# Performance work log

Hardware: AMD Instinct MI355X
Metric: run time of the kernel (lower is better)

Reference implementation:

```python
import jax, jax.numpy as jnp
import numpy as np

# Config matching init_kwargs: input_shape=(C,T,H,W)=(512,32,14,14), window_size=9, n_heads=8
B, C, T, H, W = 2, 512, 32, 14, 14
N, K = 8, 9
CI = C // N              # per-head inter channels (64)
P = (K - 1) // 2         # symmetric temporal zero-pad so S == T


def setup_inputs() -> dict:
    key = jax.random.key(0)
    ks = jax.random.split(key, 7)
    s = 0.02
    return {
        "x":  jax.random.normal(ks[0], (B, C, T, H, W), jnp.float32),
        # per-head 1x1x1 conv (Linear3d) weights/biases, stacked over heads
        "Wq": jax.random.normal(ks[1], (N, CI, C), jnp.float32) * s,
        "bq": jax.random.normal(ks[2], (N, CI), jnp.float32) * s,
        "Wk": jax.random.normal(ks[3], (N, CI, C), jnp.float32) * s,
        "bk": jax.random.normal(ks[4], (N, CI), jnp.float32) * s,
        "Wv": jax.random.normal(ks[5], (N, CI, C), jnp.float32) * s,
        "bv": jax.random.normal(ks[6], (N, CI), jnp.float32) * s,
    }


def reference(x, Wq, bq, Wk, bk, Wv, bv):
    # x: (B, C, T, H, W). Dropout (p=0.25) is inference-mode identity.
    Bx, Cx, Tx, Hx, Wd = x.shape
    HW = Hx * Wd
    xf = x.reshape(Bx, Cx, Tx, HW)

    # Queries: every original frame is the center of its own window -> project x directly.
    q = jnp.einsum('bctp,nic->bnitp', xf, Wq) + bq[None, :, :, None, None]  # (B,N,ci,T,HW)

    # Keys/values on temporally zero-padded input (Pad3d gives S == T windows).
    xp = jnp.pad(xf, ((0, 0), (0, 0), (P, P), (0, 0)))  # (B,C,T+K-1,HW)
    k = jnp.einsum('bctp,nic->bnitp', xp, Wk) + bk[None, :, :, None, None]
    v = jnp.einsum('bctp,nic->bnitp', xp, Wv) + bv[None, :, :, None, None]

    # Sliding windows over padded time: window s covers padded frames s..s+K-1
    win = jnp.arange(Tx)[:, None] + jnp.arange(K)[None, :]  # (T,K)
    kw = k[:, :, :, win]  # (B,N,ci,T,K,HW)
    vw = v[:, :, :, win].reshape(Bx, N, CI, Tx, K * HW)

    # alpha[b,n,t,p,m] = sum_i q[b,n,i,t,p] * k_win[b,n,i,t,m]; softmax over keys m
    alpha = jnp.einsum('bnitp,bnitkm->bntpkm', q, kw).reshape(Bx, N, Tx, HW, K * HW)
    alpha = jax.nn.softmax(alpha, axis=-1)

    # y = alpha @ value -> (B,N,ci,T,HW); head concat is channel-major reshape
    y = jnp.einsum('bntpm,bnitm->bnitp', alpha, vw)
    z = y.reshape(Bx, Cx, Tx, Hx, Wd) + x  # residual
    return z
```

## Files before the change

kernel.cpp:

```cpp
#include <hip/hip_runtime.h>
#include <hip/hip_bf16.h>
#include <stdint.h>
#include <cstddef>

#define BB  2
#define CC  512
#define TT  32
#define HWP 196
#define NH  8
#define KWIN 9
#define CID 64
#define PPAD 4
#define TP  40
#define MTOT 12544
#define NTOT 1536
#define VSLOT 224
#define LOG2E 1.44269504f

typedef unsigned short u16;
typedef unsigned int   u32;
typedef __attribute__((ext_vector_type(8))) short short8;
typedef __attribute__((ext_vector_type(4))) float floatx4;

__device__ __forceinline__ u16 f2bf(float f) {
    u32 u = __float_as_uint(f);
    u32 r = (u + 0x7fffu + ((u >> 16) & 1u)) >> 16;
    return (u16)r;
}
__device__ __forceinline__ u32 pack2bf(float a, float b) {
    return (u32)f2bf(a) | ((u32)f2bf(b) << 16);
}
__device__ __forceinline__ u32 packtrunc(float a, float b) {
    return __builtin_amdgcn_perm(__float_as_uint(b), __float_as_uint(a), 0x07060302u);
}
__device__ __forceinline__ float fexp2(float x) {
    return __builtin_amdgcn_exp2f(x);
}
__device__ __forceinline__ void gload16(const u16* g, u16* l) {
    __builtin_amdgcn_global_load_lds(
        (const __attribute__((address_space(1))) u32*)g,
        (__attribute__((address_space(3))) u32*)l, 16, 0, 0);
}

__global__ __launch_bounds__(256) void prep_transpose(
    const float* __restrict__ x, u16* __restrict__ xt,
    const float* __restrict__ Wq, const float* __restrict__ Wk,
    const float* __restrict__ Wv, u16* __restrict__ Wbf,
    const float* __restrict__ bk, const float* __restrict__ bv,
    u16* __restrict__ Kout, u16* __restrict__ Vtp)
{
    __shared__ float T[64 * 197];
    int bxg = blockIdx.x;
    int tid = threadIdx.x;

    if (bxg < BB * TT * 8) {
        int bx = bxg;
        int ct = bx & 7; bx >>= 3;
        int t = bx & 31;
        int b = bx >> 5;
        const float* src = x + ((size_t)(b * CC + ct * 64) * TT + t) * HWP;
        for (int i = tid; i < 64 * 49; i += 256) {
            int c = i / 49;
            int p4 = i - c * 49;
            float4 v = *(const float4*)(src + (size_t)c * (TT * HWP) + p4 * 4);
            float* Tp = &T[c * 197 + p4 * 4];
            Tp[0] = v.x; Tp[1] = v.y; Tp[2] = v.z; Tp[3] = v.w;
        }
        __syncthreads();
        u16* dst = xt + (size_t)((b * TT + t) * HWP) * CC + ct * 64;
        for (int i = tid; i < HWP * 8; i += 256) {
            int p = i >> 3;
            int c0 = (i & 7) * 8;
            u32 w[4];
            #pragma unroll
            for (int k = 0; k < 4; k++)
                w[k] = pack2bf(T[(c0 + 2 * k) * 197 + p],
                               T[(c0 + 2 * k + 1) * 197 + p]);
            *(uint4*)(dst + (size_t)p * CC + c0) = *(uint4*)w;
        }
        return;
    }

    int id = (bxg - BB * TT * 8) * 256 + tid;
    const int wtot = NTOT * CC / 2;
    const int kper = 2 * NH * 8 * HWP * 32;
    const int vper = 2 * NH * 8 * 64 * (VSLOT/2);
    if (id < wtot) {
        int c2 = id & 255;
        int oc = id >> 8;
        int kind = oc >> 9;
        int idx = oc & 511;
        const float* src = (kind == 0 ? Wq : (kind == 1 ? Wk : Wv)) + (size_t)idx * CC + c2 * 2;
        ((u32*)Wbf)[id] = pack2bf(src[0], src[1]);
    } else if (id < wtot + kper) {
        int i = id - wtot;
        int ci2 = i & 31; i >>= 5;
        int p = i % HWP;  i /= HWP;
        int fr = i & 7;   i >>= 3;
        int head = i & 7;
        int b = i >> 3;
        int tp = fr < 4 ? fr : fr + 32;
        const float* bias = bk + head * CID + ci2 * 2;
        size_t addr = (((size_t)(b * NH + head) * TP + tp) * HWP + p) * 32 + ci2;
        ((u32*)Kout)[addr] = pack2bf(bias[0], bias[1]);
    } else if (id < wtot + kper + vper) {
        int i = id - wtot - kper;
        int s2 = i % (VSLOT/2); i /= (VSLOT/2);
        int ci = i & 63; i >>= 6;
        int fr = i & 7;  i >>= 3;
        int head = i & 7;
        int b = i >> 3;
        int tp = fr < 4 ? fr : fr + 32;
        float bias = bv[head * CID + ci];
        size_t addr = (((size_t)(b * NH + head) * TP + tp) * 64 + ci) * (VSLOT/2) + s2;
        ((u32*)Vtp)[addr] = pack2bf(bias, bias);
    }
}

__global__ __launch_bounds__(512) void proj_gemm2(
    const u16* __restrict__ xt, const u16* __restrict__ Wbf,
    const float* __restrict__ bq, const float* __restrict__ bk,
    const float* __restrict__ bv,
    u16* __restrict__ Qout, u16* __restrict__ Kout, u16* __restrict__ Vtp)
{
    __shared__ u16 sA[128 * 64];
    __shared__ u16 sB[256 * 64];

    int bx = blockIdx.x;
    int nb = bx % 6;
    int mt = bx / 6;
    int tid = threadIdx.x;
    int wave = tid >> 6, lane = tid & 63, quad = lane >> 4, l15 = lane & 15;
    int wm = wave >> 2, wn = wave & 3;
    int mbase = mt * 128 + wm * 64;
    int nbase = nb * 256 + wn * 64;

    int lr = lane >> 3;
    int sw = ((lane & 7) * 8) ^ (lr << 3);

    floatx4 acc[4][4];
    #pragma unroll
    for (int ms = 0; ms < 4; ms++)
        #pragma unroll
        for (int ns = 0; ns < 4; ns++)
            acc[ms][ns] = (floatx4){0.f, 0.f, 0.f, 0.f};

    const u16* abase = xt + (size_t)(mt * 128) * CC;
    const u16* bbase = Wbf + (size_t)(nb * 256) * CC;

    for (int kc = 0; kc < 8; kc++) {
        __syncthreads();
        #pragma unroll
        for (int i = 0; i < 2; i++) {
            int rbase = wave * 16 + i * 8;
            gload16(abase + (size_t)(rbase + lr) * CC + kc * 64 + sw,
                    &sA[rbase * 64]);
        }
        #pragma unroll
        for (int i = 0; i < 4; i++) {
            int rbase = wave * 32 + i * 8;
            gload16(bbase + (size_t)(rbase + lr) * CC + kc * 64 + sw,
                    &sB[rbase * 64]);
        }
        __syncthreads();

        #pragma unroll
        for (int kk = 0; kk < 2; kk++) {
            int swr = (kk * 32 + quad * 8) ^ ((l15 & 7) << 3);
            short8 af[4], bf[4];
            #pragma unroll
            for (int ms = 0; ms < 4; ms++)
                af[ms] = *(const short8*)&sA[(wm * 64 + ms * 16 + l15) * 64 + swr];
            #pragma unroll
            for (int ns = 0; ns < 4; ns++)
                bf[ns] = *(const short8*)&sB[(wn * 64 + ns * 16 + l15) * 64 + swr];
            #pragma unroll
            for (int ms = 0; ms < 4; ms++)
                #pragma unroll
                for (int ns = 0; ns < 4; ns++)
                    acc[ms][ns] = __builtin_amdgcn_mfma_f32_16x16x32_bf16(
                        af[ms], bf[ns], acc[ms][ns], 0, 0, 0);
        }
    }

    float biasv[4];
    #pragma unroll
    for (int ns = 0; ns < 4; ns++) {
        int n = nbase + ns * 16 + l15;
        int kind = n >> 9;
        int idx = n & 511;
        const float* bpb = kind == 0 ? bq : (kind == 1 ? bk : bv);
        biasv[ns] = bpb[idx];
    }

    #pragma unroll
    for (int ms = 0; ms < 4; ms++) {
        #pragma unroll
        for (int r = 0; r < 4; r++) {
            int m = mbase + ms * 16 + quad * 4 + r;
            int b = m / (TT * HWP);
            int rem = m - b * (TT * HWP);
            int t = rem / HWP;
            int p = rem - t * HWP;
            int slot_p = (p & ~31) | (p & 3) | (((p >> 4) & 1) << 2)
                       | (((p >> 2) & 1) << 3) | (((p >> 3) & 1) << 4);
            #pragma unroll
            for (int ns = 0; ns < 4; ns++) {
                int n = nbase + ns * 16 + l15;
                int kind = n >> 9;
                int idx = n & 511;
                int head = idx >> 6;
                int ci = idx & 63;
                float val = acc[ms][ns][r] + biasv[ns];
                if (kind == 0) {
                    Qout[(((size_t)(b * NH + head) * TT + t) * HWP + p) * CID + ci]
                        = f2bf(val * LOG2E);
                } else if (kind == 1) {
                    Kout[(((size_t)(b * NH + head) * TP + (t + PPAD)) * HWP + p) * CID + ci]
                        = f2bf(val);
                } else {
                    Vtp[(((size_t)(b * NH + head) * TP + (t + PPAD)) * 64 + ci) * VSLOT + slot_p]
                        = f2bf(val);
                }
            }
        }
    }
}

__global__ __launch_bounds__(512, 1) void attn_mfma4(
    const float* __restrict__ x,
    const u16* __restrict__ Qb, const u16* __restrict__ Kb,
    const u16* __restrict__ Vtp, float* __restrict__ zout)
{
    __shared__ union {
        struct { u16 K[26 * 512]; u16 V[28 * 512]; } s;
        struct { float eT[192 * 66]; float eT12[4][4][66]; float ls12[4][4]; } e;
    } u;

    int i = blockIdx.x;
    int xcd = i & 7;
    int r = i >> 3;
    int slab = ((r >= 16) ? 8 : 0) | xcd;
    int tpair = r & 15;
    int t0 = tpair * 2;
    int b = slab >> 3, n = slab & 7;

    int tid = threadIdx.x;
    int wave = tid >> 6;
    int grp = wave >> 2;
    int wq = wave & 3;
    int t = t0 + grp;
    int lane = tid & 63;
    int quad = lane >> 4, l15 = lane & 15;
    int lr = lane >> 3;
    int ksw = ((lane & 7) * 8) ^ (lr << 3);

    const u16* kfr0 = Kb + (size_t)slab * (TP * HWP) * CID;
    const u16* vslab = Vtp + (size_t)slab * (TP * 64 * VSLOT);
    const float tmask = (quad == 0) ? 1.0f : 0.0f;

    short8 qf[3][2];
    #pragma unroll
    for (int j = 0; j < 3; j++) {
        int qrow = (wq + 4 * j) * 16 + l15;
        const u16* qp = Qb + ((size_t)(slab * TT + t) * HWP + qrow) * CID;
        qf[j][0] = *(const short8*)(qp + quad * 8);
        qf[j][1] = *(const short8*)(qp + 32 + quad * 8);
    }
    short8 qf12[2];
    {
        int qrow = 192 + l15;
        qrow = qrow < HWP ? qrow : (HWP - 1);
        const u16* qp = Qb + ((size_t)(slab * TT + t) * HWP + qrow) * CID;
        qf12[0] = *(const short8*)(qp + quad * 8);
        qf12[1] = *(const short8*)(qp + 32 + quad * 8);
    }

    floatx4 acc[3][4];
    floatx4 accl[3];
    floatx4 acc12[4];
    floatx4 accl12;
    #pragma unroll
    for (int j = 0; j < 3; j++) {
        #pragma unroll
        for (int cg = 0; cg < 4; cg++) acc[j][cg] = (floatx4){0.f, 0.f, 0.f, 0.f};
        accl[j] = (floatx4){0.f, 0.f, 0.f, 0.f};
    }
    #pragma unroll
    for (int cg = 0; cg < 4; cg++) acc12[cg] = (floatx4){0.f, 0.f, 0.f, 0.f};
    accl12 = (floatx4){0.f, 0.f, 0.f, 0.f};

    union { u32 w[4]; short8 s; } ones;
    ones.w[0] = 0x3F803F80u; ones.w[1] = 0x3F803F80u;
    ones.w[2] = 0x3F803F80u; ones.w[3] = 0x3F803F80u;

    #define KLOAD_L(c, D00, D01, D10, D11) do {                                  \
        int r0_ = (c) * 32 + l15;                                                \
        int sx_ = (l15 & 7) << 3;                                                \
        const u16* a0_ = &u.s.K[r0_ * 64];                                       \
        const u16* a1_ = &u.s.K[(r0_ + 16) * 64];                                \
        D00 = *(const short8*)(a0_ + ((quad * 8) ^ sx_));                        \
        D01 = *(const short8*)(a0_ + ((32 + quad * 8) ^ sx_));                   \
        D10 = *(const short8*)(a1_ + ((quad * 8) ^ sx_));                        \
        D11 = *(const short8*)(a1_ + ((32 + quad * 8) ^ sx_));                   \
    } while (0)

    #define KLOADTAIL_L(D00, D01) do {                                           \
        int r0_ = 192 + l15;                                                     \
        int sx_ = (l15 & 7) << 3;                                                \
        const u16* a0_ = &u.s.K[r0_ * 64];                                       \
        D00 = *(const short8*)(a0_ + ((quad * 8) ^ sx_));                        \
        D01 = *(const short8*)(a0_ + ((32 + quad * 8) ^ sx_));                   \
    } while (0)

    #define VLOAD_L(c, D0, D1, D2, D3) do {                                      \
        const u16* v_ = &u.s.V[l15 * VSLOT + (c) * 32 + quad * 8];               \
        D0 = *(const short8*)(v_);                                               \
        D1 = *(const short8*)(v_ + 16 * VSLOT);                                  \
        D2 = *(const short8*)(v_ + 32 * VSLOT);                                  \
        D3 = *(const short8*)(v_ + 48 * VSLOT);                                  \
    } while (0)

    #define CHUNK_ONE(Q0, Q1, ACC, ACCL, K00, K01, K10, K11, V0, V1, V2, V3) do {\
        floatx4 sc0 = (floatx4){0.f, 0.f, 0.f, 0.f};                             \
        sc0 = __builtin_amdgcn_mfma_f32_16x16x32_bf16(K00, Q0, sc0, 0, 0, 0);    \
        sc0 = __builtin_amdgcn_mfma_f32_16x16x32_bf16(K01, Q1, sc0, 0, 0, 0);    \
        floatx4 sc1 = (floatx4){0.f, 0.f, 0.f, 0.f};                             \
        sc1 = __builtin_amdgcn_mfma_f32_16x16x32_bf16(K10, Q0, sc1, 0, 0, 0);    \
        sc1 = __builtin_amdgcn_mfma_f32_16x16x32_bf16(K11, Q1, sc1, 0, 0, 0);    \
        union { u32 w[4]; short8 s; } pf;                                        \
        pf.w[0] = packtrunc(fexp2(sc0[0]), fexp2(sc0[1]));                       \
        pf.w[1] = packtrunc(fexp2(sc0[2]), fexp2(sc0[3]));                       \
        pf.w[2] = packtrunc(fexp2(sc1[0]), fexp2(sc1[1]));                       \
        pf.w[3] = packtrunc(fexp2(sc1[2]), fexp2(sc1[3]));                       \
        ACC[0] = __builtin_amdgcn_mfma_f32_16x16x32_bf16(pf.s, V0, ACC[0], 0, 0, 0); \
        ACC[1] = __builtin_amdgcn_mfma_f32_16x16x32_bf16(pf.s, V1, ACC[1], 0, 0, 0); \
        ACC[2] = __builtin_amdgcn_mfma_f32_16x16x32_bf16(pf.s, V2, ACC[2], 0, 0, 0); \
        ACC[3] = __builtin_amdgcn_mfma_f32_16x16x32_bf16(pf.s, V3, ACC[3], 0, 0, 0); \
        ACCL   = __builtin_amdgcn_mfma_f32_16x16x32_bf16(pf.s, ones.s, ACCL, 0, 0, 0); \
    } while (0)

    #define TAIL_ONE(Q0, Q1, ACC, ACCL, K00, K01, V0, V1, V2, V3) do {           \
        floatx4 sc0 = (floatx4){0.f, 0.f, 0.f, 0.f};                             \
        sc0 = __builtin_amdgcn_mfma_f32_16x16x32_bf16(K00, Q0, sc0, 0, 0, 0);    \
        sc0 = __builtin_amdgcn_mfma_f32_16x16x32_bf16(K01, Q1, sc0, 0, 0, 0);    \
        union { u32 w[4]; short8 s; } pf;                                        \
        pf.w[0] = packtrunc(fexp2(sc0[0]) * tmask, fexp2(sc0[1]) * tmask);       \
        pf.w[1] = packtrunc(fexp2(sc0[2]) * tmask, fexp2(sc0[3]) * tmask);       \
        pf.w[2] = 0u;                                                            \
        pf.w[3] = 0u;                                                            \
        ACC[0] = __builtin_amdgcn_mfma_f32_16x16x32_bf16(pf.s, V0, ACC[0], 0, 0, 0); \
        ACC[1] = __builtin_amdgcn_mfma_f32_16x16x32_bf16(pf.s, V1, ACC[1], 0, 0, 0); \
        ACC[2] = __builtin_amdgcn_mfma_f32_16x16x32_bf16(pf.s, V2, ACC[2], 0, 0, 0); \
        ACC[3] = __builtin_amdgcn_mfma_f32_16x16x32_bf16(pf.s, V3, ACC[3], 0, 0, 0); \
        ACCL   = __builtin_amdgcn_mfma_f32_16x16x32_bf16(pf.s, ones.s, ACCL, 0, 0, 0); \
    } while (0)

    #define CHUNK_FULL(K00, K01, K10, K11, V0, V1, V2, V3) do {                  \
        _Pragma("unroll")                                                        \
        for (int j = 0; j < 3; j++)                                              \
            CHUNK_ONE(qf[j][0], qf[j][1], acc[j], accl[j],                       \
                      K00, K01, K10, K11, V0, V1, V2, V3);                       \
        if (do12)                                                                \
            CHUNK_ONE(qf12[0], qf12[1], acc12, accl12,                           \
                      K00, K01, K10, K11, V0, V1, V2, V3);                       \
    } while (0)

    #define CHUNK_TAIL(K00, K01, V0, V1, V2, V3) do {                            \
        _Pragma("unroll")                                                        \
        for (int j = 0; j < 3; j++)                                              \
            TAIL_ONE(qf[j][0], qf[j][1], acc[j], accl[j],                        \
                     K00, K01, V0, V1, V2, V3);                                  \
        if (do12)                                                                \
            TAIL_ONE(qf12[0], qf12[1], acc12, accl12,                            \
                     K00, K01, V0, V1, V2, V3);                                  \
    } while (0)

    for (int fa = 0; fa < KWIN + 1; fa++) {
        int af = t0 + fa;
        const u16* kfr = kfr0 + (size_t)(af * HWP) * CID;
        const u16* vfr = vslab + (size_t)af * (64 * VSLOT);

        __syncthreads();
        #pragma unroll
        for (int it = 0; it < 7; it++) {
            int idx = it * 8 + wave;
            if (idx < 26) {
                gload16(kfr + (size_t)(idx * 8 + lr) * CID + ksw,
                        &u.s.K[idx * 512]);
            } else if (idx < 54) {
                int j2 = idx - 26;
                gload16(vfr + j2 * 512 + lane * 8, &u.s.V[j2 * 512]);
            }
        }
        __syncthreads();

        bool active = (grp == 0) ? (fa < KWIN) : (fa >= 1);
        int fr = fa - grp;
        if (active) {
            bool do12 = ((fr & 3) == wq);
            #pragma unroll
            for (int c = 0; c < 6; c++) {
                short8 k00, k01, k10, k11, v0, v1, v2, v3;
                KLOAD_L(c, k00, k01, k10, k11);
                VLOAD_L(c, v0, v1, v2, v3);
                CHUNK_FULL(k00, k01, k10, k11, v0, v1, v2, v3);
            }
            {
                short8 k00, k01, v0, v1, v2, v3;
                KLOADTAIL_L(k00, k01);
                VLOAD_L(6, v0, v1, v2, v3);
                CHUNK_TAIL(k00, k01, v0, v1, v2, v3);
            }
        }
    }

    #undef KLOAD_L
    #undef KLOADTAIL_L
    #undef VLOAD_L
    #undef CHUNK_ONE
    #undef TAIL_ONE
    #undef CHUNK_FULL
    #undef CHUNK_TAIL

    __syncthreads();

    #pragma unroll
    for (int ph = 0; ph < 2; ph++) {
        if (grp == ph) {
            #pragma unroll
            for (int j = 0; j < 3; j++) {
                int tg = wq + 4 * j;
                float il[4];
                #pragma unroll
                for (int rr = 0; rr < 4; rr++) il[rr] = 1.0f / accl[j][rr];
                #pragma unroll
                for (int cg = 0; cg < 4; cg++) {
                    #pragma unroll
                    for (int rr = 0; rr < 4; rr++) {
                        int p = tg * 16 + quad * 4 + rr;
                        u.e.eT[p * 66 + cg * 16 + l15] = acc[j][cg][rr] * il[rr];
                    }
                }
            }
            if (quad == 0) {
                #pragma unroll
                for (int rr = 0; rr < 4; rr++) {
                    #pragma unroll
                    for (int cg = 0; cg < 4; cg++)
                        u.e.eT12[wq][rr][cg * 16 + l15] = acc12[cg][rr];
                    if (l15 == 0) u.e.ls12[wq][rr] = accl12[rr];
                }
            }
        }
        __syncthreads();

        {
            int p = tid >> 1;
            int ch = tid & 1;
            if (p < HWP) {
                size_t base = ((size_t)(b * CC + n * CID + ch * 32) * TT
                               + (t0 + ph)) * HWP + p;
                if (p < 192) {
                    for (int ci = 0; ci < 32; ci++) {
                        size_t a = base + (size_t)ci * (TT * HWP);
                        zout[a] = u.e.eT[p * 66 + ch * 32 + ci] + x[a];
                    }
                } else {
                    int rr = p - 192;
                    float l = u.e.ls12[0][rr] + u.e.ls12[1][rr]
                            + u.e.ls12[2][rr] + u.e.ls12[3][rr];
                    float il = 1.0f / l;
                    for (int ci = 0; ci < 32; ci++) {
                        size_t a = base + (size_t)ci * (TT * HWP);
                        int cc = ch * 32 + ci;
                        float v = (u.e.eT12[0][rr][cc] + u.e.eT12[1][rr][cc]
                                 + u.e.eT12[2][rr][cc] + u.e.eT12[3][rr][cc]) * il;
                        zout[a] = v + x[a];
                    }
                }
            }
        }
        __syncthreads();
    }
}

extern "C" void kernel_launch(void* const* d_in, const int* in_sizes, int n_in,
                              void* d_out, int out_size, void* d_ws, size_t ws_size,
                              hipStream_t stream) {
    const float* x  = (const float*)d_in[0];
    const float* Wq = (const float*)d_in[1];
    const float* bq = (const float*)d_in[2];
    const float* Wk = (const float*)d_in[3];
    const float* bk = (const float*)d_in[4];
    const float* Wv = (const float*)d_in[5];
    const float* bv = (const float*)d_in[6];
    float* z = (float*)d_out;

    const size_t qElems   = (size_t)BB * NH * TT * HWP * CID;
    const size_t kElems   = (size_t)BB * NH * TP * HWP * CID;
    const size_t vtpElems = (size_t)BB * NH * TP * 64 * VSLOT;

    u16* Qw  = (u16*)d_ws;
    u16* Kw  = Qw + qElems;
    u16* Vtp = Kw + kElems;
    u16* Wb  = Vtp + vtpElems;
    u16* Xt  = (u16*)d_out;

    {
        const int wtot = NTOT * CC / 2;
        const int kper = 2 * NH * 8 * HWP * 32;
        const int vper = 2 * NH * 8 * 64 * (VSLOT / 2);
        const int prepBlocks = (wtot + kper + vper + 255) / 256;
        prep_transpose<<<BB * TT * 8 + prepBlocks, 256, 0, stream>>>(
            x, Xt, Wq, Wk, Wv, Wb, bk, bv, Kw, Vtp);
    }
    proj_gemm2<<<98 * 6, 512, 0, stream>>>(Xt, Wb, bq, bk, bv, Qw, Kw, Vtp);
    attn_mfma4<<<256, 512, 0, stream>>>(x, Qw, Kw, Vtp, z);
}
```

Before: 215.4 us.

## Double-buffer K/V frame staging in shared memory for attention kernel

Replaces the single static LDS buffer with two dynamic-shared-memory buffers so the K/V tiles for the next frame are issued while the current frame is computed. This drops one barrier per frame and overlaps global-to-LDS loads with the MFMA/exp work. It doubles LDS use to about 110 KB per block, which needs a raised dynamic shared memory attribute. The epilogue reuses the same buffer through pointer aliasing.

Measured after the change: 214.3 us. No clear change (-0.5%).

```diff
diff --git a/kernel.cpp b/kernel.cpp
--- a/kernel.cpp
+++ b/kernel.cpp
@@ -16,6 +16,10 @@
 #define NTOT 1536
 #define VSLOT 224
 #define LOG2E 1.44269504f
+
+#define KBUF_U16 13312
+#define VBUF_U16 14336
+#define BUF_U16  27648
 
 typedef unsigned short u16;
 typedef unsigned int   u32;
@@ -232,10 +236,7 @@
     const u16* __restrict__ Qb, const u16* __restrict__ Kb,
     const u16* __restrict__ Vtp, float* __restrict__ zout)
 {
-    __shared__ union {
-        struct { u16 K[26 * 512]; u16 V[28 * 512]; } s;
-        struct { float eT[192 * 66]; float eT12[4][4][66]; float ls12[4][4]; } e;
-    } u;
+    extern __shared__ u16 smem[];
 
     int i = blockIdx.x;
     int xcd = i & 7;
@@ -294,27 +295,45 @@
     ones.w[0] = 0x3F803F80u; ones.w[1] = 0x3F803F80u;
     ones.w[2] = 0x3F803F80u; ones.w[3] = 0x3F803F80u;
 
-    #define KLOAD_L(c, D00, D01, D10, D11) do {                                  \
+    #define STAGE(af_, bb_) do {                                                 \
+        const u16* kfr_ = kfr0 + (size_t)((af_) * HWP) * CID;                    \
+        const u16* vfr_ = vslab + (size_t)(af_) * (64 * VSLOT);                  \
+        u16* kb_ = smem + (bb_) * BUF_U16;                                       \
+        u16* vb_ = kb_ + KBUF_U16;                                               \
+        _Pragma("unroll")                                                        \
+        for (int it = 0; it < 7; it++) {                                         \
+            int idx = it * 8 + wave;                                             \
+            if (idx < 26) {                                                      \
+                gload16(kfr_ + (size_t)(idx * 8 + lr) * CID + ksw,               \
+                        kb_ + idx * 512);                                        \
+            } else if (idx < 54) {                                               \
+                int j2_ = idx - 26;                                              \
+                gload16(vfr_ + j2_ * 512 + lane * 8, vb_ + j2_ * 512);           \
+            }                                                                    \
+        }                                                                        \
+    } while (0)
+
+    #define KLOAD_L(kb_, c, D00, D01, D10, D11) do {                             \
         int r0_ = (c) * 32 + l15;                                                \
         int sx_ = (l15 & 7) << 3;                                                \
-        const u16* a0_ = &u.s.K[r0_ * 64];                                       \
-        const u16* a1_ = &u.s.K[(r0_ + 16) * 64];                                \
+        const u16* a0_ = kb_ + r0_ * 64;                                         \
+        const u16* a1_ = kb_ + (r0_ + 16) * 64;                                  \
         D00 = *(const short8*)(a0_ + ((quad * 8) ^ sx_));                        \
         D01 = *(const short8*)(a0_ + ((32 + quad * 8) ^ sx_));                   \
         D10 = *(const short8*)(a1_ + ((quad * 8) ^ sx_));                        \
         D11 = *(const short8*)(a1_ + ((32 + quad * 8) ^ sx_));                   \
     } while (0)
 
-    #define KLOADTAIL_L(D00, D01) do {                                           \
+    #define KLOADTAIL_L(kb_, D00, D01) do {                                      \
         int r0_ = 192 + l15;                                                     \
         int sx_ = (l15 & 7) << 3;                                                \
-        const u16* a0_ = &u.s.K[r0_ * 64];                                       \
+        const u16* a0_ = kb_ + r0_ * 64;                                         \
         D00 = *(const short8*)(a0_ + ((quad * 8) ^ sx_));                        \
         D01 = *(const short8*)(a0_ + ((32 + quad * 8) ^ sx_));                   \
     } while (0)
 
-    #define VLOAD_L(c, D0, D1, D2, D3) do {                                      \
-        const u16* v_ = &u.s.V[l15 * VSLOT + (c) * 32 + quad * 8];               \
+    #define VLOAD_L(vb_, c, D0, D1, D2, D3) do {                                 \
+        const u16* v_ = vb_ + l15 * VSLOT + (c) * 32 + quad * 8;                 \
         D0 = *(const short8*)(v_);                                               \
         D1 = *(const short8*)(v_ + 16 * VSLOT);                                  \
         D2 = *(const short8*)(v_ + 32 * VSLOT);                                  \
@@ -376,45 +395,36 @@
                      K00, K01, V0, V1, V2, V3);                                  \
     } while (0)
 
+    STAGE(t0, 0);
+    __syncthreads();
+
     for (int fa = 0; fa < KWIN + 1; fa++) {
-        int af = t0 + fa;
-        const u16* kfr = kfr0 + (size_t)(af * HWP) * CID;
-        const u16* vfr = vslab + (size_t)af * (64 * VSLOT);
-
-        __syncthreads();
-        #pragma unroll
-        for (int it = 0; it < 7; it++) {
-            int idx = it * 8 + wave;
-            if (idx < 26) {
-                gload16(kfr + (size_t)(idx * 8 + lr) * CID + ksw,
-                        &u.s.K[idx * 512]);
-            } else if (idx < 54) {
-                int j2 = idx - 26;
-                gload16(vfr + j2 * 512 + lane * 8, &u.s.V[j2 * 512]);
-            }
-        }
-        __syncthreads();
+        if (fa + 1 < KWIN + 1) STAGE(t0 + fa + 1, (fa + 1) & 1);
 
         bool active = (grp == 0) ? (fa < KWIN) : (fa >= 1);
         int fr = fa - grp;
+        const u16* kb = smem + (fa & 1) * BUF_U16;
+        const u16* vb = kb + KBUF_U16;
         if (active) {
             bool do12 = ((fr & 3) == wq);
             #pragma unroll
             for (int c = 0; c < 6; c++) {
                 short8 k00, k01, k10, k11, v0, v1, v2, v3;
-                KLOAD_L(c, k00, k01, k10, k11);
-                VLOAD_L(c, v0, v1, v2, v3);
+                KLOAD_L(kb, c, k00, k01, k10, k11);
+                VLOAD_L(vb, c, v0, v1, v2, v3);
                 CHUNK_FULL(k00, k01, k10, k11, v0, v1, v2, v3);
             }
             {
                 short8 k00, k01, v0, v1, v2, v3;
-                KLOADTAIL_L(k00, k01);
-                VLOAD_L(6, v0, v1, v2, v3);
+                KLOADTAIL_L(kb, k00, k01);
+                VLOAD_L(vb, 6, v0, v1, v2, v3);
                 CHUNK_TAIL(k00, k01, v0, v1, v2, v3);
             }
         }
-    }
-
+        __syncthreads();
+    }
+
+    #undef STAGE
     #undef KLOAD_L
     #undef KLOADTAIL_L
     #undef VLOAD_L
@@ -423,7 +433,9 @@
     #undef CHUNK_FULL
     #undef CHUNK_TAIL
 
-    __syncthreads();
+    float* eT   = (float*)smem;
+    float* eT12 = eT + 192 * 66;
+    float* ls12 = eT12 + 4 * 4 * 66;
 
     #pragma unroll
     for (int ph = 0; ph < 2; ph++) {
@@ -439,7 +451,7 @@
                     #pragma unroll
                     for (int rr = 0; rr < 4; rr++) {
                         int p = tg * 16 + quad * 4 + rr;
-                        u.e.eT[p * 66 + cg * 16 + l15] = acc[j][cg][rr] * il[rr];
+                        eT[p * 66 + cg * 16 + l15] = acc[j][cg][rr] * il[rr];
                     }
                 }
             }
@@ -448,8 +460,8 @@
                 for (int rr = 0; rr < 4; rr++) {
                     #pragma unroll
                     for (int cg = 0; cg < 4; cg++)
-                        u.e.eT12[wq][rr][cg * 16 + l15] = acc12[cg][rr];
-                    if (l15 == 0) u.e.ls12[wq][rr] = accl12[rr];
+                        eT12[(wq * 4 + rr) * 66 + cg * 16 + l15] = acc12[cg][rr];
+                    if (l15 == 0) ls12[wq * 4 + rr] = accl12[rr];
                 }
             }
         }
@@ -464,18 +476,17 @@
                 if (p < 192) {
                     for (int ci = 0; ci < 32; ci++) {
                         size_t a = base + (size_t)ci * (TT * HWP);
-                        zout[a] = u.e.eT[p * 66 + ch * 32 + ci] + x[a];
+                        zout[a] = eT[p * 66 + ch * 32 + ci] + x[a];
                     }
                 } else {
                     int rr = p - 192;
-                    float l = u.e.ls12[0][rr] + u.e.ls12[1][rr]
-                            + u.e.ls12[2][rr] + u.e.ls12[3][rr];
+                    float l = ls12[rr] + ls12[4 + rr] + ls12[8 + rr] + ls12[12 + rr];
                     float il = 1.0f / l;
                     for (int ci = 0; ci < 32; ci++) {
                         size_t a = base + (size_t)ci * (TT * HWP);
                         int cc = ch * 32 + ci;
-                        float v = (u.e.eT12[0][rr][cc] + u.e.eT12[1][rr][cc]
-                                 + u.e.eT12[2][rr][cc] + u.e.eT12[3][rr][cc]) * il;
+                        float v = (eT12[rr * 66 + cc] + eT12[(4 + rr) * 66 + cc]
+                                 + eT12[(8 + rr) * 66 + cc] + eT12[(12 + rr) * 66 + cc]) * il;
                         zout[a] = v + x[a];
                     }
                 }
@@ -507,6 +518,14 @@
     u16* Wb  = Vtp + vtpElems;
     u16* Xt  = (u16*)d_out;
 
+    static bool attrDone = false;
+    if (!attrDone) {
+        hipFuncSetAttribute((const void*)attn_mfma4,
+                            hipFuncAttributeMaxDynamicSharedMemorySize,
+                            2 * BUF_U16 * 2);
+        attrDone = true;
+    }
+
     {
         const int wtot = NTOT * CC / 2;
         const int kper = 2 * NH * 8 * HWP * 32;
@@ -516,5 +535,5 @@
             x, Xt, Wq, Wk, Wv, Wb, bk, bv, Kw, Vtp);
     }
     proj_gemm2<<<98 * 6, 512, 0, stream>>>(Xt, Wb, bq, bk, bv, Qw, Kw, Vtp);
-    attn_mfma4<<<256, 512, 0, stream>>>(x, Qw, Kw, Vtp, z);
-}
+    attn_mfma4<<<256, 512, 2 * BUF_U16 * 2, stream>>>(x, Qw, Kw, Vtp, z);
+}
```
